# Performance work log

Measured on AMD Instinct MI355X. Metric: run time of the kernel, lower is better.

## Reference

```python
import jax, jax.numpy as jnp
import numpy as np

B, T, D, H = 1, 2049, 1024, 16
HD = D // H                      # head_dim = 64
MAX_SEQ = 1025
L = 2 * MAX_SEQ - 1              # = T (required by the module's relative shift)

def setup_inputs() -> dict:
    key = jax.random.key(0)
    ks = jax.random.split(key, 12)
    s = 0.02
    return {
        'q': jax.random.normal(ks[0], (B, T, D), dtype=jnp.float32),
        'k': jax.random.normal(ks[1], (B, T, D), dtype=jnp.float32),
        'v': jax.random.normal(ks[2], (B, T, D), dtype=jnp.float32),
        'mask': jnp.tril(jnp.ones((1, 1, T, T), dtype=jnp.int32)),  # causal
        'Wq_w': jax.random.normal(ks[3], (D, D), dtype=jnp.float32) * s,
        'Wq_b': jnp.zeros((D,), dtype=jnp.float32),
        'Wk_w': jax.random.normal(ks[4], (D, D), dtype=jnp.float32) * s,
        'Wk_b': jnp.zeros((D,), dtype=jnp.float32),
        'Wv_w': jax.random.normal(ks[5], (D, D), dtype=jnp.float32) * s,
        'Wv_b': jnp.zeros((D,), dtype=jnp.float32),
        'Er': jax.random.normal(ks[6], (L, HD), dtype=jnp.float32),
        'Wo_w': jax.random.normal(ks[7], (D, D), dtype=jnp.float32) * s,
        'Wo_b': jnp.zeros((D,), dtype=jnp.float32),
    }

def reference(q, k, v, mask, Wq_w, Wq_b, Wk_w, Wk_b, Wv_w, Wv_b, Er, Wo_w, Wo_b):
    b, t, d = q.shape
    def proj(x, w, bias):
        # nn.Linear: x @ W^T + b ; then (B,T,H,HD) -> (B,H,T,HD)
        return (x @ w.T + bias).reshape(b, t, H, HD).transpose(0, 2, 1, 3)
    qh = proj(q, Wq_w, Wq_b)
    kh = proj(k, Wk_w, Wk_b)
    vh = proj(v, Wv_w, Wv_b)
    scores = jnp.einsum('bhtd,bhsd->bhts', qh, kh)          # (B,H,T,T)
    QEr = jnp.einsum('bhtd,ld->bhtl', qh, Er)               # (B,H,T,L) with L == T
    # _relative_shift: pad a zero row on seq dim then drop first row ->
    # row i becomes QEr row i+1, last row zeros (faithful to torch code)
    rel = jnp.concatenate([QEr[:, :, 1:, :], jnp.zeros_like(QEr[:, :, :1, :])], axis=2)
    scores = scores + rel
    scores = jnp.where(mask[:, :, :t, :t] == 0, -jnp.inf, scores)
    attn = jax.nn.softmax(scores / (HD ** 0.5), axis=-1)
    ctx = jnp.einsum('bhts,bhsd->bthd', attn, vh).reshape(b, t, d)
    return ctx @ Wo_w.T + Wo_b
```

## Files before the change

### kernel.cpp

```cpp
#include <hip/hip_runtime.h>
#include <hip/hip_bf16.h>
#include <math.h>

constexpr int T_SEQ = 2049;
constexpr int D_MODEL = 1024;
constexpr int N_HEAD = 16;
constexpr int HEAD_DIM = 64;
constexpr int VT_STRIDE = 2112;
constexpr int T1_ROWS = 1152;

typedef __attribute__((ext_vector_type(8))) short short8;
typedef __attribute__((ext_vector_type(4))) short short4v;
typedef __attribute__((ext_vector_type(4))) float floatx4;

__device__ inline void load_lds16(const void* g, void* l) {
  __builtin_amdgcn_global_load_lds(
      (const __attribute__((address_space(1))) unsigned int*)g,
      (__attribute__((address_space(3))) unsigned int*)l, 16, 0, 0);
}

__device__ inline short8 cvt8_bf16(const float* p) {
  float4 a = *(const float4*)p, b = *(const float4*)(p + 4);
  __hip_bfloat16 t[8] = {__float2bfloat16(a.x), __float2bfloat16(a.y),
                         __float2bfloat16(a.z), __float2bfloat16(a.w),
                         __float2bfloat16(b.x), __float2bfloat16(b.y),
                         __float2bfloat16(b.z), __float2bfloat16(b.w)};
  return *(const short8*)t;
}

__device__ inline float bf2f(__hip_bfloat16 x) { return __bfloat162float(x); }

__global__ __launch_bounds__(256) void cast_all(
    const float* __restrict__ q, const float* __restrict__ k,
    const float* __restrict__ v, const float* __restrict__ wq,
    const float* __restrict__ wk, const float* __restrict__ wv,
    const float* __restrict__ er, const float* __restrict__ wo,
    __hip_bfloat16* __restrict__ qo, __hip_bfloat16* __restrict__ ko,
    __hip_bfloat16* __restrict__ vo, __hip_bfloat16* __restrict__ wqo,
    __hip_bfloat16* __restrict__ wko, __hip_bfloat16* __restrict__ wvo,
    __hip_bfloat16* __restrict__ ero, __hip_bfloat16* __restrict__ woo) {
  const int z = blockIdx.y;
  const float* in;
  __hip_bfloat16* out;
  int n;
  switch (z) {
    case 0: in = q; out = qo; n = T_SEQ * D_MODEL; break;
    case 1: in = k; out = ko; n = T_SEQ * D_MODEL; break;
    case 2: in = v; out = vo; n = T_SEQ * D_MODEL; break;
    case 3: in = wq; out = wqo; n = D_MODEL * D_MODEL; break;
    case 4: in = wk; out = wko; n = D_MODEL * D_MODEL; break;
    case 5: in = wv; out = wvo; n = D_MODEL * D_MODEL; break;
    case 6: in = er; out = ero; n = T_SEQ * HEAD_DIM; break;
    default: in = wo; out = woo; n = D_MODEL * D_MODEL; break;
  }
  const int i = (blockIdx.x * 256 + threadIdx.x) * 8;
  if (i + 8 > n) return;
  *(short8*)(out + i) = cvt8_bf16(in + i);
}

__global__ __launch_bounds__(512) void qkv_gemm8(
    const __hip_bfloat16* __restrict__ qbf, const __hip_bfloat16* __restrict__ kbf,
    const __hip_bfloat16* __restrict__ vbf, const __hip_bfloat16* __restrict__ wqb,
    const __hip_bfloat16* __restrict__ wkb, const __hip_bfloat16* __restrict__ wvb,
    const float* __restrict__ bq, const float* __restrict__ bk,
    const float* __restrict__ bv, __hip_bfloat16* __restrict__ qpr,
    __hip_bfloat16* __restrict__ kpr, __hip_bfloat16* __restrict__ vt,
    const float* __restrict__ er, __hip_bfloat16* __restrict__ er_bf) {
  const int d = blockIdx.x;
  const int tid = threadIdx.x;
  if (d >= 408) {
    const int i = ((d - 408) * 512 + tid) * 8;
    if (i + 8 <= T_SEQ * HEAD_DIM) *(short8*)(er_bf + i) = cvt8_bf16(er + i);
    return;
  }
  int x, p;
  if (d < 384) {
    const int g = d >> 6, rem = d & 63;
    x = rem >> 3;
    p = g * 8 + (rem & 7);
  } else {
    const int t = d - 384;
    p = 48 + (t >> 3);
    x = t & 7;
  }
  const int y = p % 17, z = p / 17;

  constexpr int K = D_MODEL, BK = 32, NS = K / BK;
  __shared__ __align__(16) char smem[32768];

  const short* A = (const short*)(z == 0 ? qbf : z == 1 ? kbf : vbf);
  const short* W = (const short*)(z == 0 ? wqb : z == 1 ? wkb : wvb);
  const float* bias = z == 0 ? bq : z == 1 ? bk : bv;

  const int wave = tid >> 6, lane = tid & 63;
  const int col = lane & 15, quad = lane >> 4;
  const int wm = wave >> 2, wn = wave & 3;
  const int m0 = y * 128, n0 = x * 128;

  const int srow = wave * 16 + (lane >> 2);
  const int sch = (lane & 3) ^ ((srow >> 1) & 3);
  const int am = min(m0 + srow, T_SEQ - 1);

#define STG(K0, BUF)                                                        \
  {                                                                         \
    load_lds16(A + (size_t)am * K + (K0) + sch * 8,                         \
               smem + (BUF)*8192 + wave * 1024);                            \
    load_lds16(W + (size_t)(n0 + srow) * K + (K0) + sch * 8,                \
               smem + 16384 + (BUF)*8192 + wave * 1024);                    \
  }

  floatx4 acc[4][2];
#pragma unroll
  for (int i = 0; i < 4; i++)
#pragma unroll
    for (int j = 0; j < 2; j++) acc[i][j] = (floatx4){0.f, 0.f, 0.f, 0.f};

  STG(0, 0)
  int buf = 0;
  for (int k0 = 0; k0 < K; k0 += BK, buf ^= 1) {
    if (k0 + BK < K) {
      STG(k0 + BK, buf ^ 1)
      asm volatile("s_waitcnt vmcnt(2)" ::: "memory");
    } else {
      asm volatile("s_waitcnt vmcnt(0)" ::: "memory");
    }
    __builtin_amdgcn_s_barrier();

    const __hip_bfloat16* as = (const __hip_bfloat16*)(smem + buf * 8192);
    const __hip_bfloat16* bs = (const __hip_bfloat16*)(smem + 16384 + buf * 8192);
    short8 af[4], bfr[2];
#pragma unroll
    for (int t = 0; t < 4; t++) {
      const int ra = wm * 64 + t * 16 + col;
      af[t] = *(const short8*)(as + ra * 32 + ((quad ^ ((ra >> 1) & 3)) * 8));
    }
#pragma unroll
    for (int t = 0; t < 2; t++) {
      const int rb = wn * 32 + t * 16 + col;
      bfr[t] = *(const short8*)(bs + rb * 32 + ((quad ^ ((rb >> 1) & 3)) * 8));
    }
#pragma unroll
    for (int mt = 0; mt < 4; mt++)
#pragma unroll
      for (int nt = 0; nt < 2; nt++)
        acc[mt][nt] = __builtin_amdgcn_mfma_f32_16x16x32_bf16(af[mt], bfr[nt],
                                                              acc[mt][nt], 0, 0, 0);
    asm volatile("" ::: "memory");
    __builtin_amdgcn_s_barrier();
  }
#undef STG

  if (z == 2) {
    short* Tt = (short*)smem;
#pragma unroll
    for (int mt = 0; mt < 4; mt++) {
      const int mb = wm * 16 + mt * 4 + quad;
#pragma unroll
      for (int nt = 0; nt < 2; nt++) {
        const int n = wn * 32 + nt * 16 + col;
        const float bb = bias[n0 + n];
        __hip_bfloat16 pk[4];
#pragma unroll
        for (int r = 0; r < 4; r++) pk[r] = __float2bfloat16(acc[mt][nt][r] + bb);
        *(short4v*)((char*)Tt + n * 256 + ((mb ^ (n & 15)) << 3)) =
            *(const short4v*)pk;
      }
    }
    __syncthreads();
    if (tid < 256) {
      const int n_loc = tid >> 1, half = tid & 1;
      if (m0 + half * 64 < VT_STRIDE) {
        const int ng = n0 + n_loc;
        __hip_bfloat16* dst = vt +
                              ((size_t)(ng >> 6) * HEAD_DIM + (ng & 63)) * VT_STRIDE +
                              m0 + half * 64;
#pragma unroll
        for (int c = 0; c < 8; c++) {
          short4v lo = *(const short4v*)((char*)Tt + n_loc * 256 +
                                         (((half * 16 + 2 * c) ^ (n_loc & 15)) << 3));
          short4v hi = *(const short4v*)((char*)Tt + n_loc * 256 +
                                         (((half * 16 + 2 * c + 1) ^ (n_loc & 15)) << 3));
          short8 o8 = {lo[0], lo[1], lo[2], lo[3], hi[0], hi[1], hi[2], hi[3]};
          *(short8*)((short*)dst + c * 8) = o8;
        }
      }
    }
    return;
  }

  __hip_bfloat16* C = z == 0 ? qpr : kpr;
#pragma unroll
  for (int mt = 0; mt < 4; mt++) {
#pragma unroll
    for (int r = 0; r < 4; r++) {
      const int m = m0 + wm * 64 + mt * 16 + quad * 4 + r;
      if (m >= T_SEQ) continue;
#pragma unroll
      for (int nt = 0; nt < 2; nt++) {
        const int n = n0 + wn * 32 + nt * 16 + col;
        const float val = acc[mt][nt][r] + bias[n];
        const int h = n >> 6, hd = n & 63;
        C[((size_t)h * T_SEQ + m) * HEAD_DIM + hd] = __float2bfloat16(val);
      }
    }
  }
}

__global__ __launch_bounds__(256) void out_gemm(
    const __hip_bfloat16* __restrict__ ctxb, const __hip_bfloat16* __restrict__ wob,
    const float* __restrict__ bias, float* __restrict__ out) {
  const int d = blockIdx.x;
  int x, p;
  if (d < 512) {
    const int g = d >> 7, rem = d & 127;
    x = rem >> 3;
    p = g * 8 + (rem & 7);
  } else {
    p = 32;
    x = d - 512;
  }
  const int m0 = p * 64, n0 = x * 64;

  constexpr int K = D_MODEL, BK = 32;
  __shared__ __align__(16) char smem[16384];

  const int tid = threadIdx.x;
  const int wave = tid >> 6, lane = tid & 63;
  const int col = lane & 15, quad = lane >> 4;
  const int wm = wave >> 1, wn = wave & 1;

  const int srow = wave * 16 + (lane >> 2);
  const int sch = (lane & 3) ^ ((srow >> 1) & 3);
  const int am = min(m0 + srow, T_SEQ - 1);
  const short* A = (const short*)ctxb;
  const short* W = (const short*)wob;

#define STG(K0, BUF)                                                        \
  {                                                                         \
    load_lds16(A + (size_t)am * K + (K0) + sch * 8,                         \
               smem + (BUF)*4096 + wave * 1024);                            \
    load_lds16(W + (size_t)(n0 + srow) * K + (K0) + sch * 8,                \
               smem + 8192 + (BUF)*4096 + wave * 1024);                     \
  }

  floatx4 acc[2][2];
#pragma unroll
  for (int i = 0; i < 2; i++)
#pragma unroll
    for (int j = 0; j < 2; j++) acc[i][j] = (floatx4){0.f, 0.f, 0.f, 0.f};

  STG(0, 0)
  int buf = 0;
  for (int k0 = 0; k0 < K; k0 += BK, buf ^= 1) {
    if (k0 + BK < K) {
      STG(k0 + BK, buf ^ 1)
      asm volatile("s_waitcnt vmcnt(2)" ::: "memory");
    } else {
      asm volatile("s_waitcnt vmcnt(0)" ::: "memory");
    }
    __builtin_amdgcn_s_barrier();

    const __hip_bfloat16* as = (const __hip_bfloat16*)(smem + buf * 4096);
    const __hip_bfloat16* bs = (const __hip_bfloat16*)(smem + 8192 + buf * 4096);
    short8 af[2], bfr[2];
#pragma unroll
    for (int t = 0; t < 2; t++) {
      const int ra = wm * 32 + t * 16 + col;
      af[t] = *(const short8*)(as + ra * 32 + ((quad ^ ((ra >> 1) & 3)) * 8));
    }
#pragma unroll
    for (int t = 0; t < 2; t++) {
      const int rb = wn * 32 + t * 16 + col;
      bfr[t] = *(const short8*)(bs + rb * 32 + ((quad ^ ((rb >> 1) & 3)) * 8));
    }
#pragma unroll
    for (int mt = 0; mt < 2; mt++)
#pragma unroll
      for (int nt = 0; nt < 2; nt++)
        acc[mt][nt] = __builtin_amdgcn_mfma_f32_16x16x32_bf16(af[mt], bfr[nt],
                                                              acc[mt][nt], 0, 0, 0);
    asm volatile("" ::: "memory");
    __builtin_amdgcn_s_barrier();
  }
#undef STG

#pragma unroll
  for (int mt = 0; mt < 2; mt++) {
#pragma unroll
    for (int r = 0; r < 4; r++) {
      const int m = m0 + wm * 32 + mt * 16 + quad * 4 + r;
      if (m >= T_SEQ) continue;
#pragma unroll
      for (int nt = 0; nt < 2; nt++) {
        const int n = n0 + wn * 32 + nt * 16 + col;
        out[(size_t)m * D_MODEL + n] = acc[mt][nt][r] + bias[n];
      }
    }
  }
}

__global__ __launch_bounds__(512, 4) void flash_attn(
    const __hip_bfloat16* __restrict__ qh, const __hip_bfloat16* __restrict__ kh,
    const __hip_bfloat16* __restrict__ er, const __hip_bfloat16* __restrict__ vt,
    __hip_bfloat16* __restrict__ ctx, __hip_bfloat16* __restrict__ O0,
    __hip_bfloat16* __restrict__ O1, float* __restrict__ l0g,
    float* __restrict__ l1g) {
  __shared__ __align__(16) __hip_bfloat16 Ks[2][64 * 128];
  __shared__ __align__(16) __hip_bfloat16 Vs[2][64 * 64];
  __shared__ __align__(16) __hip_bfloat16 Ps[8][1024];

  const int tid = threadIdx.x;
  const int id = blockIdx.x + 26 * blockIdx.y;
  const int slot = id >> 3;
  const int h = (id & 7) + 8 * (slot >= 26);
  const int b = 25 - (slot >= 26 ? slot - 26 : slot);

  const int qt = (b < 8) ? b : 8 + ((b - 8) >> 1);
  const int tq0 = qt * 128;
  const int jmax = min(tq0 + 127, T_SEQ - 1) >> 6;
  int j0, j1;
  bool alt;
  if (b < 8) {
    j0 = 0; j1 = jmax; alt = false;
  } else {
    const int mid = (jmax + 1) >> 1;
    alt = (b - 8) & 1;
    j0 = alt ? mid : 0;
    j1 = alt ? jmax : mid - 1;
  }

  const int wave = tid >> 6;
  const int lane = tid & 63;
  const int col = lane & 15;
  const int quad = lane >> 4;

  const short* qplane = (const short*)(qh + (size_t)h * T_SEQ * HEAD_DIM);
  const short* kplane = (const short*)(kh + (size_t)h * T_SEQ * HEAD_DIM);
  const short* eplane = (const short*)er;
  const short* vplane = (const short*)(vt + (size_t)h * HEAD_DIM * VT_STRIDE);

  const int t_abs = tq0 + wave * 16 + col;
  const int tload = min(t_abs, T_SEQ - 1);
  const bool hiz = (t_abs >= T_SEQ - 1);
  short8 aq[4];
#pragma unroll
  for (int kc = 0; kc < 4; kc++) {
    short8 v = *(const short8*)(qplane + (size_t)tload * 64 + kc * 32 + quad * 8);
    if (kc >= 2 && hiz) v = (short8){0, 0, 0, 0, 0, 0, 0, 0};
    aq[kc] = v;
  }

  floatx4 o[4];
  float l_lane = 0.f;
#pragma unroll
  for (int i = 0; i < 4; i++) o[i] = (floatx4){0.f, 0.f, 0.f, 0.f};

  const int tstrip = tq0 + wave * 16;
  __hip_bfloat16* psw = &Ps[wave][0];

#define STAGE_TILE(JJ, BUF)                                                        \
  {                                                                                \
    const int s0_ = (JJ) * 64;                                                     \
    _Pragma("unroll") for (int ii = 0; ii < 2; ii++) {                             \
      const int i_ = wave * 2 + ii;                                                \
      const int r_ = i_ * 4 + (lane >> 4);                                         \
      const int sl_ = lane & 15;                                                   \
      const int g_ = (sl_ & 8) | ((sl_ ^ (r_ & 7)) & 7);                           \
      const int s_ = min(s0_ + r_, T_SEQ - 1);                                     \
      const short* src_ = (g_ < 8) ? (kplane + (size_t)s_ * 64 + g_ * 8)           \
                                   : (eplane + (size_t)s_ * 64 + (g_ - 8) * 8);    \
      load_lds16(src_, (char*)&Ks[BUF][0] + i_ * 1024);                            \
    }                                                                              \
    {                                                                              \
      const int d_ = wave * 8 + (lane >> 3);                                       \
      const int sl_ = lane & 7;                                                    \
      const int g_ = sl_ ^ (d_ & 7);                                               \
      load_lds16(vplane + (size_t)d_ * VT_STRIDE + s0_ + g_ * 8,                   \
                 (char*)&Vs[BUF][0] + wave * 1024);                                \
    }                                                                              \
  }

  STAGE_TILE(j0, 0)
  int buf = 0;

  for (int j = j0; j <= j1; ++j, buf ^= 1) {
    __syncthreads();
    if (j < j1) STAGE_TILE(j + 1, buf ^ 1)

    const int s0 = j * 64;
    if (s0 > tstrip + 15) continue;

    const __hip_bfloat16* ks = &Ks[buf][0];
    const __hip_bfloat16* vs = &Vs[buf][0];

    floatx4 sacc[4];
    __builtin_amdgcn_s_setprio(1);
#pragma unroll
    for (int st = 0; st < 4; st++) {
      floatx4 c = {0.f, 0.f, 0.f, 0.f};
      const int row = st * 16 + col;
#pragma unroll
      for (int kc = 0; kc < 4; kc++) {
        const int ch = kc * 4 + quad;
        const int slot2 = (ch & 8) | ((ch ^ (row & 7)) & 7);
        short8 ka = *(const short8*)(ks + row * 128 + slot2 * 8);
        c = __builtin_amdgcn_mfma_f32_16x16x32_bf16(ka, aq[kc], c, 0, 0, 0);
      }
      sacc[st] = c;
    }
    __builtin_amdgcn_s_setprio(0);

    if (s0 + 63 > tstrip) {
#pragma unroll
      for (int st = 0; st < 4; st++) {
        const int sbase = s0 + st * 16 + quad * 4;
#pragma unroll
        for (int r = 0; r < 4; r++)
          if (sbase + r > t_abs) sacc[st][r] = -INFINITY;
      }
    }

    float rs = 0.f;
#pragma unroll
    for (int st = 0; st < 4; st++)
#pragma unroll
      for (int r = 0; r < 4; r++) {
        const float pql = __expf(sacc[st][r] * 0.125f);
        sacc[st][r] = pql;
        rs += pql;
      }
    l_lane += rs;

#pragma unroll
    for (int st = 0; st < 4; st++) {
      __hip_bfloat16 pb[4];
#pragma unroll
      for (int r = 0; r < 4; r++) pb[r] = __float2bfloat16(sacc[st][r]);
      const int kcA = st >> 1;
      const int quadA = (st & 1) * 2 + (quad >> 1);
      const int off = ((kcA * 4 + quadA) * 16 + col) * 8 + (quad & 1) * 4;
      *(short4v*)(psw + off) = *(const short4v*)pb;
    }
    short8 pa[2];
#pragma unroll
    for (int kc = 0; kc < 2; kc++)
      pa[kc] = *(const short8*)(psw + ((kc * 4 + quad) * 16 + col) * 8);

    __builtin_amdgcn_s_setprio(1);
#pragma unroll
    for (int nt = 0; nt < 4; nt++) {
      const int row = nt * 16 + col;
#pragma unroll
      for (int kc = 0; kc < 2; kc++) {
        const int slot2 = (kc * 4 + quad) ^ (row & 7);
        short8 vb = *(const short8*)(vs + row * 64 + slot2 * 8);
        o[nt] = __builtin_amdgcn_mfma_f32_16x16x32_bf16(pa[kc], vb, o[nt], 0, 0, 0);
      }
    }
    __builtin_amdgcn_s_setprio(0);
  }

  l_lane += __shfl_xor(l_lane, 16, 64);
  l_lane += __shfl_xor(l_lane, 32, 64);

  if (b < 8) {
    const float linv = 1.0f / l_lane;
    float linv_r[4];
#pragma unroll
    for (int r = 0; r < 4; r++) linv_r[r] = __shfl(linv, quad * 4 + r, 64);
#pragma unroll
    for (int r = 0; r < 4; r++) {
      const int t = tstrip + quad * 4 + r;
#pragma unroll
      for (int nt = 0; nt < 4; nt++)
        ctx[(size_t)t * D_MODEL + h * 64 + nt * 16 + col] =
            __float2bfloat16(o[nt][r] * linv_r[r]);
    }
  } else {
    if (lane < 16) {
      const int t = tstrip + lane;
      if (t < T_SEQ) {
        if (!alt)
          l0g[h * T1_ROWS + (t - 1024)] = l_lane;
        else
          l1g[h * T1_ROWS + (t - 1024)] = l_lane;
      }
    }
#pragma unroll
    for (int r = 0; r < 4; r++) {
      const int t = tstrip + quad * 4 + r;
      if (t < T_SEQ) {
        __hip_bfloat16* dst = (!alt ? O0 : O1) + (size_t)(t - 1024) * D_MODEL;
#pragma unroll
        for (int nt = 0; nt < 4; nt++)
          dst[h * 64 + nt * 16 + col] = __float2bfloat16(o[nt][r]);
      }
    }
  }
}

__global__ __launch_bounds__(256) void finalize(
    const __hip_bfloat16* __restrict__ O0, const __hip_bfloat16* __restrict__ O1,
    const float* __restrict__ l0g, const float* __restrict__ l1g,
    __hip_bfloat16* __restrict__ ctx) {
  const int idx = blockIdx.x * 256 + threadIdx.x;
  const int tr = idx >> 7;
  const int t = 1024 + tr;
  if (t >= T_SEQ) return;
  const int ch = idx & 127;
  const int h = ch >> 3;

  const float l = l0g[h * T1_ROWS + tr] + l1g[h * T1_ROWS + tr];
  const __hip_bfloat16* a = O0 + (size_t)tr * D_MODEL + ch * 8;
  const __hip_bfloat16* bsrc = O1 + (size_t)tr * D_MODEL + ch * 8;
  const float inv = 1.0f / l;
  __hip_bfloat16 outv[8];
#pragma unroll
  for (int i = 0; i < 8; i++)
    outv[i] = __float2bfloat16((bf2f(a[i]) + bf2f(bsrc[i])) * inv);
  *(short8*)(ctx + (size_t)t * D_MODEL + ch * 8) = *(const short8*)outv;
}

extern "C" void kernel_launch(void* const* d_in, const int* in_sizes, int n_in,
                              void* d_out, int out_size, void* d_ws, size_t ws_size,
                              hipStream_t stream) {
  const float* q = (const float*)d_in[0];
  const float* k = (const float*)d_in[1];
  const float* v = (const float*)d_in[2];
  const float* Wq_w = (const float*)d_in[4];
  const float* Wq_b = (const float*)d_in[5];
  const float* Wk_w = (const float*)d_in[6];
  const float* Wk_b = (const float*)d_in[7];
  const float* Wv_w = (const float*)d_in[8];
  const float* Wv_b = (const float*)d_in[9];
  const float* Er = (const float*)d_in[10];
  const float* Wo_w = (const float*)d_in[11];
  const float* Wo_b = (const float*)d_in[12];
  float* out = (float*)d_out;

  char* ws = (char*)d_ws;
  const size_t sz_plane = (size_t)T_SEQ * D_MODEL * 2;
  const size_t sz_w = (size_t)D_MODEL * D_MODEL * 2;
  const size_t sz_vt = (size_t)N_HEAD * HEAD_DIM * VT_STRIDE * 2;
  const size_t sz_er = (size_t)T_SEQ * HEAD_DIM * 2;
  const size_t sz_Op = (size_t)T1_ROWS * D_MODEL * 2;
  const size_t sz_l = (size_t)N_HEAD * T1_ROWS * 4;

  __hip_bfloat16* qbf = (__hip_bfloat16*)ws;
  __hip_bfloat16* kbf = (__hip_bfloat16*)(ws + sz_plane);
  __hip_bfloat16* vbf = (__hip_bfloat16*)(ws + 2 * sz_plane);
  __hip_bfloat16* wqb = (__hip_bfloat16*)(ws + 3 * sz_plane);
  __hip_bfloat16* wkb = (__hip_bfloat16*)(ws + 3 * sz_plane + sz_w);
  __hip_bfloat16* wvb = (__hip_bfloat16*)(ws + 3 * sz_plane + 2 * sz_w);
  char* hi = ws + 3 * sz_plane + 3 * sz_w;
  __hip_bfloat16* qpr = (__hip_bfloat16*)hi;
  __hip_bfloat16* kpr = (__hip_bfloat16*)(hi + sz_plane);
  __hip_bfloat16* vt = (__hip_bfloat16*)(hi + 2 * sz_plane);
  __hip_bfloat16* er_bf = (__hip_bfloat16*)(hi + 2 * sz_plane + sz_vt);
  __hip_bfloat16* wob = (__hip_bfloat16*)(hi + 2 * sz_plane + sz_vt + sz_er);

  __hip_bfloat16* ctxb = (__hip_bfloat16*)ws;
  __hip_bfloat16* O0 = (__hip_bfloat16*)(ws + sz_plane);
  __hip_bfloat16* O1 = (__hip_bfloat16*)(ws + sz_plane + sz_Op);
  float* l0g = (float*)(ws + sz_plane + 2 * sz_Op);
  float* l1g = (float*)(ws + sz_plane + 2 * sz_Op + sz_l);

  const dim3 blk(256);

  cast_all<<<dim3(1025, 8), blk, 0, stream>>>(q, k, v, Wq_w, Wk_w, Wv_w, Er, Wo_w,
                                              qbf, kbf, vbf, wqb, wkb, wvb, er_bf,
                                              wob);

  qkv_gemm8<<<dim3(441), dim3(512), 0, stream>>>(
      qbf, kbf, vbf, wqb, wkb, wvb, Wq_b, Wk_b, Wv_b, qpr, kpr, vt, Er, er_bf);

  flash_attn<<<dim3(26, N_HEAD), dim3(512), 0, stream>>>(qpr, kpr, er_bf, vt, ctxb,
                                                         O0, O1, l0g, l1g);

  finalize<<<dim3((1025 * 128 + 255) / 256), blk, 0, stream>>>(O0, O1, l0g, l1g,
                                                               ctxb);

  out_gemm<<<dim3(528), blk, 0, stream>>>(ctxb, wob, Wo_b, out);
}
```

Before: 180.8 us.

## Fuse split-KV finalize into flash attention via atomic ticket merge

Removes the separate finalize kernel. Each split-KV flash-attention block takes an atomic ticket per (head, query tile), and the second block to finish combines its partial output with the other block's stored partial and normalizer, then writes ctx directly. Ticket reset is folded into the cast kernel, and the redundant Er conversion blocks are dropped from the QKV GEMM launch. This saves one kernel launch and a pass over the partial buffers, in exchange for a threadfence, an atomic and extra tail work in the last-finishing blocks.

Measured after the change: 269.3 us. +49.0%, slower.

```diff
diff --git a/kernel.cpp b/kernel.cpp
--- a/kernel.cpp
+++ b/kernel.cpp
@@ -8,6 +8,7 @@
 constexpr int HEAD_DIM = 64;
 constexpr int VT_STRIDE = 2112;
 constexpr int T1_ROWS = 1152;
+constexpr int N_TICKETS = 144;
 
 typedef __attribute__((ext_vector_type(8))) short short8;
 typedef __attribute__((ext_vector_type(4))) short short4v;
@@ -38,7 +39,8 @@
     __hip_bfloat16* __restrict__ qo, __hip_bfloat16* __restrict__ ko,
     __hip_bfloat16* __restrict__ vo, __hip_bfloat16* __restrict__ wqo,
     __hip_bfloat16* __restrict__ wko, __hip_bfloat16* __restrict__ wvo,
-    __hip_bfloat16* __restrict__ ero, __hip_bfloat16* __restrict__ woo) {
+    __hip_bfloat16* __restrict__ ero, __hip_bfloat16* __restrict__ woo,
+    int* __restrict__ tickets) {
   const int z = blockIdx.y;
   const float* in;
   __hip_bfloat16* out;
@@ -50,7 +52,11 @@
     case 3: in = wq; out = wqo; n = D_MODEL * D_MODEL; break;
     case 4: in = wk; out = wko; n = D_MODEL * D_MODEL; break;
     case 5: in = wv; out = wvo; n = D_MODEL * D_MODEL; break;
-    case 6: in = er; out = ero; n = T_SEQ * HEAD_DIM; break;
+    case 6:
+      if (blockIdx.x == 1024 && threadIdx.x < N_TICKETS)
+        tickets[threadIdx.x] = 0;
+      in = er; out = ero; n = T_SEQ * HEAD_DIM;
+      break;
     default: in = wo; out = woo; n = D_MODEL * D_MODEL; break;
   }
   const int i = (blockIdx.x * 256 + threadIdx.x) * 8;
@@ -64,15 +70,9 @@
     const __hip_bfloat16* __restrict__ wkb, const __hip_bfloat16* __restrict__ wvb,
     const float* __restrict__ bq, const float* __restrict__ bk,
     const float* __restrict__ bv, __hip_bfloat16* __restrict__ qpr,
-    __hip_bfloat16* __restrict__ kpr, __hip_bfloat16* __restrict__ vt,
-    const float* __restrict__ er, __hip_bfloat16* __restrict__ er_bf) {
+    __hip_bfloat16* __restrict__ kpr, __hip_bfloat16* __restrict__ vt) {
   const int d = blockIdx.x;
   const int tid = threadIdx.x;
-  if (d >= 408) {
-    const int i = ((d - 408) * 512 + tid) * 8;
-    if (i + 8 <= T_SEQ * HEAD_DIM) *(short8*)(er_bf + i) = cvt8_bf16(er + i);
-    return;
-  }
   int x, p;
   if (d < 384) {
     const int g = d >> 6, rem = d & 63;
@@ -85,7 +85,7 @@
   }
   const int y = p % 17, z = p / 17;
 
-  constexpr int K = D_MODEL, BK = 32, NS = K / BK;
+  constexpr int K = D_MODEL, BK = 32;
   __shared__ __align__(16) char smem[32768];
 
   const short* A = (const short*)(z == 0 ? qbf : z == 1 ? kbf : vbf);
@@ -304,10 +304,11 @@
     const __hip_bfloat16* __restrict__ er, const __hip_bfloat16* __restrict__ vt,
     __hip_bfloat16* __restrict__ ctx, __hip_bfloat16* __restrict__ O0,
     __hip_bfloat16* __restrict__ O1, float* __restrict__ l0g,
-    float* __restrict__ l1g) {
+    float* __restrict__ l1g, int* __restrict__ tickets) {
   __shared__ __align__(16) __hip_bfloat16 Ks[2][64 * 128];
   __shared__ __align__(16) __hip_bfloat16 Vs[2][64 * 64];
   __shared__ __align__(16) __hip_bfloat16 Ps[8][1024];
+  __shared__ int sold;
 
   const int tid = threadIdx.x;
   const int id = blockIdx.x + 26 * blockIdx.y;
@@ -479,46 +480,53 @@
   } else {
     if (lane < 16) {
       const int t = tstrip + lane;
-      if (t < T_SEQ) {
-        if (!alt)
-          l0g[h * T1_ROWS + (t - 1024)] = l_lane;
-        else
-          l1g[h * T1_ROWS + (t - 1024)] = l_lane;
-      }
+      if (t < T_SEQ)
+        (alt ? l1g : l0g)[h * T1_ROWS + (t - 1024)] = l_lane;
     }
 #pragma unroll
     for (int r = 0; r < 4; r++) {
       const int t = tstrip + quad * 4 + r;
       if (t < T_SEQ) {
-        __hip_bfloat16* dst = (!alt ? O0 : O1) + (size_t)(t - 1024) * D_MODEL;
+        __hip_bfloat16* dst = (alt ? O1 : O0) + (size_t)(t - 1024) * D_MODEL;
 #pragma unroll
         for (int nt = 0; nt < 4; nt++)
           dst[h * 64 + nt * 16 + col] = __float2bfloat16(o[nt][r]);
       }
     }
-  }
-}
-
-__global__ __launch_bounds__(256) void finalize(
-    const __hip_bfloat16* __restrict__ O0, const __hip_bfloat16* __restrict__ O1,
-    const float* __restrict__ l0g, const float* __restrict__ l1g,
-    __hip_bfloat16* __restrict__ ctx) {
-  const int idx = blockIdx.x * 256 + threadIdx.x;
-  const int tr = idx >> 7;
-  const int t = 1024 + tr;
-  if (t >= T_SEQ) return;
-  const int ch = idx & 127;
-  const int h = ch >> 3;
-
-  const float l = l0g[h * T1_ROWS + tr] + l1g[h * T1_ROWS + tr];
-  const __hip_bfloat16* a = O0 + (size_t)tr * D_MODEL + ch * 8;
-  const __hip_bfloat16* bsrc = O1 + (size_t)tr * D_MODEL + ch * 8;
-  const float inv = 1.0f / l;
-  __hip_bfloat16 outv[8];
-#pragma unroll
-  for (int i = 0; i < 8; i++)
-    outv[i] = __float2bfloat16((bf2f(a[i]) + bf2f(bsrc[i])) * inv);
-  *(short8*)(ctx + (size_t)t * D_MODEL + ch * 8) = *(const short8*)outv;
+    __threadfence();
+    __syncthreads();
+    if (tid == 0) sold = atomicAdd(&tickets[h * 9 + (qt - 8)], 1);
+    __syncthreads();
+    if (sold == 1) {
+      __threadfence();
+      const float* lother = alt ? l0g : l1g;
+      const __hip_bfloat16* Oother = alt ? O0 : O1;
+      float lt = 1.f;
+      {
+        const int t = tstrip + col;
+        if (t < T_SEQ) lt = l_lane + lother[h * T1_ROWS + (t - 1024)];
+      }
+      const float linv = 1.0f / lt;
+      float linv_r[4];
+#pragma unroll
+      for (int r = 0; r < 4; r++) linv_r[r] = __shfl(linv, quad * 4 + r, 64);
+#pragma unroll
+      for (int r = 0; r < 4; r++) {
+        const int t = tstrip + quad * 4 + r;
+        if (t < T_SEQ) {
+          const __hip_bfloat16* osrc = Oother + (size_t)(t - 1024) * D_MODEL;
+#pragma unroll
+          for (int nt = 0; nt < 4; nt++) {
+            const int c = h * 64 + nt * 16 + col;
+            const float own = bf2f(__float2bfloat16(o[nt][r]));
+            const float oth = bf2f(osrc[c]);
+            ctx[(size_t)t * D_MODEL + c] =
+                __float2bfloat16((own + oth) * linv_r[r]);
+          }
+        }
+      }
+    }
+  }
 }
 
 extern "C" void kernel_launch(void* const* d_in, const int* in_sizes, int n_in,
@@ -558,6 +566,7 @@
   __hip_bfloat16* vt = (__hip_bfloat16*)(hi + 2 * sz_plane);
   __hip_bfloat16* er_bf = (__hip_bfloat16*)(hi + 2 * sz_plane + sz_vt);
   __hip_bfloat16* wob = (__hip_bfloat16*)(hi + 2 * sz_plane + sz_vt + sz_er);
+  int* tickets = (int*)(hi + 2 * sz_plane + sz_vt + sz_er + sz_w);
 
   __hip_bfloat16* ctxb = (__hip_bfloat16*)ws;
   __hip_bfloat16* O0 = (__hip_bfloat16*)(ws + sz_plane);
@@ -569,16 +578,13 @@
 
   cast_all<<<dim3(1025, 8), blk, 0, stream>>>(q, k, v, Wq_w, Wk_w, Wv_w, Er, Wo_w,
                                               qbf, kbf, vbf, wqb, wkb, wvb, er_bf,
-                                              wob);
-
-  qkv_gemm8<<<dim3(441), dim3(512), 0, stream>>>(
-      qbf, kbf, vbf, wqb, wkb, wvb, Wq_b, Wk_b, Wv_b, qpr, kpr, vt, Er, er_bf);
-
-  flash_attn<<<dim3(26, N_HEAD), dim3(512), 0, stream>>>(qpr, kpr, er_bf, vt, ctxb,
-                                                         O0, O1, l0g, l1g);
-
-  finalize<<<dim3((1025 * 128 + 255) / 256), blk, 0, stream>>>(O0, O1, l0g, l1g,
-                                                               ctxb);
+                                              wob, tickets);
+
+  qkv_gemm8<<<dim3(408), dim3(512), 0, stream>>>(
+      qbf, kbf, vbf, wqb, wkb, wvb, Wq_b, Wk_b, Wv_b, qpr, kpr, vt);
+
+  flash_attn<<<dim3(26, N_HEAD), dim3(512), 0, stream>>>(
+      qpr, kpr, er_bf, vt, ctxb, O0, O1, l0g, l1g, tickets);
 
   out_gemm<<<dim3(528), blk, 0, stream>>>(ctxb, wob, Wo_b, out);
 }
```

## Fuse split-KV finalize merge into output projection GEMM A-tile loading

Applied to the files above, without the earlier changes.

Removes the separate finalize kernel and instead has out_gemm blocks covering rows >= 1024 load both partial attention outputs and their row sums directly. These blocks normalize and convert the partials in registers, then write them to LDS through a register-staged software pipeline. This removes one launch and the ctx write/read round trip for the second half of rows. In exchange, those blocks use synchronous register loads instead of async global-to-LDS loads and read two planes plus the l arrays redundantly for each N tile.

New measurement: 185.5 us. 1.03x slower.

```diff
diff --git a/kernel.cpp b/kernel.cpp
--- a/kernel.cpp
+++ b/kernel.cpp
@@ -85,7 +85,7 @@
   }
   const int y = p % 17, z = p / 17;
 
-  constexpr int K = D_MODEL, BK = 32, NS = K / BK;
+  constexpr int K = D_MODEL, BK = 32;
   __shared__ __align__(16) char smem[32768];
 
   const short* A = (const short*)(z == 0 ? qbf : z == 1 ? kbf : vbf);
@@ -207,7 +207,9 @@
 }
 
 __global__ __launch_bounds__(256) void out_gemm(
-    const __hip_bfloat16* __restrict__ ctxb, const __hip_bfloat16* __restrict__ wob,
+    const __hip_bfloat16* __restrict__ ctxb, const __hip_bfloat16* __restrict__ O0,
+    const __hip_bfloat16* __restrict__ O1, const float* __restrict__ l0g,
+    const float* __restrict__ l1g, const __hip_bfloat16* __restrict__ wob,
     const float* __restrict__ bias, float* __restrict__ out) {
   const int d = blockIdx.x;
   int x, p;
@@ -220,8 +222,9 @@
     x = d - 512;
   }
   const int m0 = p * 64, n0 = x * 64;
-
-  constexpr int K = D_MODEL, BK = 32;
+  const bool merge = (m0 >= 1024);
+
+  constexpr int K = D_MODEL, BK = 32, NS = K / BK;
   __shared__ __align__(16) char smem[16384];
 
   const int tid = threadIdx.x;
@@ -232,9 +235,16 @@
   const int srow = wave * 16 + (lane >> 2);
   const int sch = (lane & 3) ^ ((srow >> 1) & 3);
   const int am = min(m0 + srow, T_SEQ - 1);
-  const short* A = (const short*)ctxb;
-  const short* W = (const short*)wob;
-
+
+  floatx4 acc[2][2];
+#pragma unroll
+  for (int i = 0; i < 2; i++)
+#pragma unroll
+    for (int j = 0; j < 2; j++) acc[i][j] = (floatx4){0.f, 0.f, 0.f, 0.f};
+
+  if (!merge) {
+    const short* A = (const short*)ctxb;
+    const short* W = (const short*)wob;
 #define STG(K0, BUF)                                                        \
   {                                                                         \
     load_lds16(A + (size_t)am * K + (K0) + sch * 8,                         \
@@ -242,47 +252,105 @@
     load_lds16(W + (size_t)(n0 + srow) * K + (K0) + sch * 8,                \
                smem + 8192 + (BUF)*4096 + wave * 1024);                     \
   }
-
-  floatx4 acc[2][2];
-#pragma unroll
-  for (int i = 0; i < 2; i++)
-#pragma unroll
-    for (int j = 0; j < 2; j++) acc[i][j] = (floatx4){0.f, 0.f, 0.f, 0.f};
-
-  STG(0, 0)
-  int buf = 0;
-  for (int k0 = 0; k0 < K; k0 += BK, buf ^= 1) {
-    if (k0 + BK < K) {
-      STG(k0 + BK, buf ^ 1)
-      asm volatile("s_waitcnt vmcnt(2)" ::: "memory");
-    } else {
-      asm volatile("s_waitcnt vmcnt(0)" ::: "memory");
-    }
-    __builtin_amdgcn_s_barrier();
-
-    const __hip_bfloat16* as = (const __hip_bfloat16*)(smem + buf * 4096);
-    const __hip_bfloat16* bs = (const __hip_bfloat16*)(smem + 8192 + buf * 4096);
-    short8 af[2], bfr[2];
-#pragma unroll
-    for (int t = 0; t < 2; t++) {
-      const int ra = wm * 32 + t * 16 + col;
-      af[t] = *(const short8*)(as + ra * 32 + ((quad ^ ((ra >> 1) & 3)) * 8));
-    }
-#pragma unroll
-    for (int t = 0; t < 2; t++) {
-      const int rb = wn * 32 + t * 16 + col;
-      bfr[t] = *(const short8*)(bs + rb * 32 + ((quad ^ ((rb >> 1) & 3)) * 8));
-    }
-#pragma unroll
-    for (int mt = 0; mt < 2; mt++)
-#pragma unroll
-      for (int nt = 0; nt < 2; nt++)
-        acc[mt][nt] = __builtin_amdgcn_mfma_f32_16x16x32_bf16(af[mt], bfr[nt],
-                                                              acc[mt][nt], 0, 0, 0);
-    asm volatile("" ::: "memory");
-    __builtin_amdgcn_s_barrier();
-  }
+    STG(0, 0)
+    int buf = 0;
+    for (int k0 = 0; k0 < K; k0 += BK, buf ^= 1) {
+      if (k0 + BK < K) {
+        STG(k0 + BK, buf ^ 1)
+        asm volatile("s_waitcnt vmcnt(2)" ::: "memory");
+      } else {
+        asm volatile("s_waitcnt vmcnt(0)" ::: "memory");
+      }
+      __builtin_amdgcn_s_barrier();
+
+      const __hip_bfloat16* as = (const __hip_bfloat16*)(smem + buf * 4096);
+      const __hip_bfloat16* bs = (const __hip_bfloat16*)(smem + 8192 + buf * 4096);
+      short8 af[2], bfr[2];
+#pragma unroll
+      for (int t = 0; t < 2; t++) {
+        const int ra = wm * 32 + t * 16 + col;
+        af[t] = *(const short8*)(as + ra * 32 + ((quad ^ ((ra >> 1) & 3)) * 8));
+      }
+#pragma unroll
+      for (int t = 0; t < 2; t++) {
+        const int rb = wn * 32 + t * 16 + col;
+        bfr[t] = *(const short8*)(bs + rb * 32 + ((quad ^ ((rb >> 1) & 3)) * 8));
+      }
+#pragma unroll
+      for (int mt = 0; mt < 2; mt++)
+#pragma unroll
+        for (int nt = 0; nt < 2; nt++)
+          acc[mt][nt] = __builtin_amdgcn_mfma_f32_16x16x32_bf16(af[mt], bfr[nt],
+                                                                acc[mt][nt], 0, 0, 0);
+      asm volatile("" ::: "memory");
+      __builtin_amdgcn_s_barrier();
+    }
 #undef STG
+  } else {
+    const int tr = am - 1024;
+    const short* O0s = (const short*)O0;
+    const short* O1s = (const short*)O1;
+    const short* Ws = (const short*)wob;
+    short8 rA0, rA1, rW, SA, SW;
+    float rl0, rl1;
+#define LOADM(K0)                                                           \
+  {                                                                         \
+    const int kb = (K0) + sch * 8;                                          \
+    rA0 = *(const short8*)(O0s + (size_t)tr * K + kb);                      \
+    rA1 = *(const short8*)(O1s + (size_t)tr * K + kb);                      \
+    rl0 = l0g[(kb >> 6) * T1_ROWS + tr];                                    \
+    rl1 = l1g[(kb >> 6) * T1_ROWS + tr];                                    \
+    rW = *(const short8*)(Ws + (size_t)(n0 + srow) * K + (K0) + sch * 8);   \
+  }
+#define CVTM()                                                              \
+  {                                                                         \
+    const float inv = 1.0f / (rl0 + rl1);                                   \
+    __hip_bfloat16 t8[8];                                                   \
+    _Pragma("unroll") for (int e = 0; e < 8; e++) t8[e] = __float2bfloat16( \
+        (bf2f(((const __hip_bfloat16*)&rA0)[e]) +                           \
+         bf2f(((const __hip_bfloat16*)&rA1)[e])) * inv);                    \
+    SA = *(const short8*)t8;                                                \
+    SW = rW;                                                                \
+  }
+    LOADM(0)
+    CVTM()
+    LOADM(BK)
+    int buf = 0;
+    for (int s = 0; s < NS; ++s, buf ^= 1) {
+      *(short8*)(smem + buf * 4096 + wave * 1024 + (lane << 4)) = SA;
+      *(short8*)(smem + 8192 + buf * 4096 + wave * 1024 + (lane << 4)) = SW;
+      asm volatile("s_waitcnt lgkmcnt(0)" ::: "memory");
+      __builtin_amdgcn_sched_barrier(0);
+      __builtin_amdgcn_s_barrier();
+
+      const __hip_bfloat16* as = (const __hip_bfloat16*)(smem + buf * 4096);
+      const __hip_bfloat16* bs = (const __hip_bfloat16*)(smem + 8192 + buf * 4096);
+      short8 af[2], bfr[2];
+#pragma unroll
+      for (int t = 0; t < 2; t++) {
+        const int ra = wm * 32 + t * 16 + col;
+        af[t] = *(const short8*)(as + ra * 32 + ((quad ^ ((ra >> 1) & 3)) * 8));
+      }
+#pragma unroll
+      for (int t = 0; t < 2; t++) {
+        const int rb = wn * 32 + t * 16 + col;
+        bfr[t] = *(const short8*)(bs + rb * 32 + ((quad ^ ((rb >> 1) & 3)) * 8));
+      }
+#pragma unroll
+      for (int mt = 0; mt < 2; mt++)
+#pragma unroll
+        for (int nt = 0; nt < 2; nt++)
+          acc[mt][nt] = __builtin_amdgcn_mfma_f32_16x16x32_bf16(af[mt], bfr[nt],
+                                                                acc[mt][nt], 0, 0, 0);
+      if (s + 1 < NS) {
+        __builtin_amdgcn_sched_barrier(0);
+        CVTM()
+        if (s + 2 < NS) LOADM((s + 2) * BK)
+      }
+    }
+#undef LOADM
+#undef CVTM
+  }
 
 #pragma unroll
   for (int mt = 0; mt < 2; mt++) {
@@ -499,28 +567,6 @@
   }
 }
 
-__global__ __launch_bounds__(256) void finalize(
-    const __hip_bfloat16* __restrict__ O0, const __hip_bfloat16* __restrict__ O1,
-    const float* __restrict__ l0g, const float* __restrict__ l1g,
-    __hip_bfloat16* __restrict__ ctx) {
-  const int idx = blockIdx.x * 256 + threadIdx.x;
-  const int tr = idx >> 7;
-  const int t = 1024 + tr;
-  if (t >= T_SEQ) return;
-  const int ch = idx & 127;
-  const int h = ch >> 3;
-
-  const float l = l0g[h * T1_ROWS + tr] + l1g[h * T1_ROWS + tr];
-  const __hip_bfloat16* a = O0 + (size_t)tr * D_MODEL + ch * 8;
-  const __hip_bfloat16* bsrc = O1 + (size_t)tr * D_MODEL + ch * 8;
-  const float inv = 1.0f / l;
-  __hip_bfloat16 outv[8];
-#pragma unroll
-  for (int i = 0; i < 8; i++)
-    outv[i] = __float2bfloat16((bf2f(a[i]) + bf2f(bsrc[i])) * inv);
-  *(short8*)(ctx + (size_t)t * D_MODEL + ch * 8) = *(const short8*)outv;
-}
-
 extern "C" void kernel_launch(void* const* d_in, const int* in_sizes, int n_in,
                               void* d_out, int out_size, void* d_ws, size_t ws_size,
                               hipStream_t stream) {
@@ -577,8 +623,5 @@
   flash_attn<<<dim3(26, N_HEAD), dim3(512), 0, stream>>>(qpr, kpr, er_bf, vt, ctxb,
                                                          O0, O1, l0g, l1g);
 
-  finalize<<<dim3((1025 * 128 + 255) / 256), blk, 0, stream>>>(O0, O1, l0g, l1g,
-                                                               ctxb);
-
-  out_gemm<<<dim3(528), blk, 0, stream>>>(ctxb, wob, Wo_b, out);
+  out_gemm<<<dim3(528), blk, 0, stream>>>(ctxb, O0, O1, l0g, l1g, wob, Wo_b, out);
 }
```

## Rebalance flash-attention work with finer split-KV partitions and table-driven scheduling

Applied to the files above, without the earlier changes.

Replaces the fixed split of query tiles (first 8 tiles whole, the rest split in two along KV) with a lookup table of 33 work slots per head. Tiles from 768 onward are split into two or three KV partitions, and the slots are issued in a chosen longest-first order. The grid grows from 26x16 to 33x16 blocks so per-block work is more even across CUs. In exchange, more rows need partial outputs written and merged, and finalize now reduces up to three partials over 1281 rows.

Measured after the change: 176.1 us. 1.03x faster.

```diff
diff --git a/kernel.cpp b/kernel.cpp
--- a/kernel.cpp
+++ b/kernel.cpp
@@ -7,11 +7,27 @@
 constexpr int N_HEAD = 16;
 constexpr int HEAD_DIM = 64;
 constexpr int VT_STRIDE = 2112;
-constexpr int T1_ROWS = 1152;
+constexpr int T2_ROWS = 1281;
 
 typedef __attribute__((ext_vector_type(8))) short short8;
 typedef __attribute__((ext_vector_type(4))) short short4v;
 typedef __attribute__((ext_vector_type(4))) float floatx4;
+
+__device__ const int d_qt[33] = {0, 1, 2, 3, 4,  5,  6,  6,  7,  7,  8,
+                                 8, 9, 9, 10, 10, 11, 11, 12, 12, 12, 13,
+                                 13, 13, 14, 14, 14, 15, 15, 15, 16, 16, 16};
+__device__ const int d_pt[33] = {0, 0, 0, 0, 0, 0, 0, 1, 0, 1, 0,
+                                 1, 0, 1, 0, 1, 0, 1, 0, 1, 2, 0,
+                                 1, 2, 0, 1, 2, 0, 1, 2, 0, 1, 2};
+__device__ const int d_j0[33] = {0, 0, 0, 0, 0,  0,  0, 7, 0, 8, 0,
+                                 9, 0, 10, 0, 11, 0, 12, 0, 8, 17, 0,
+                                 9, 18, 0, 10, 20, 0, 10, 21, 0, 11, 22};
+__device__ const int d_j1[33] = {1, 3, 5, 7, 9,  11, 6, 13, 7, 15, 8,
+                                 17, 9, 19, 10, 21, 11, 23, 7, 16, 25, 8,
+                                 17, 27, 9, 19, 29, 9, 20, 31, 10, 21, 32};
+__device__ const int d_ord[33] = {5, 16, 17, 14, 15, 28, 29, 30, 31, 32, 4,
+                                  12, 13, 23, 24, 25, 26, 27, 10, 11, 19, 20,
+                                  21, 22, 3, 8, 9, 18, 6, 7, 2, 1, 0};
 
 __device__ inline void load_lds16(const void* g, void* l) {
   __builtin_amdgcn_global_load_lds(
@@ -85,7 +101,7 @@
   }
   const int y = p % 17, z = p / 17;
 
-  constexpr int K = D_MODEL, BK = 32, NS = K / BK;
+  constexpr int K = D_MODEL, BK = 32;
   __shared__ __align__(16) char smem[32768];
 
   const short* A = (const short*)(z == 0 ? qbf : z == 1 ? kbf : vbf);
@@ -302,32 +318,23 @@
 __global__ __launch_bounds__(512, 4) void flash_attn(
     const __hip_bfloat16* __restrict__ qh, const __hip_bfloat16* __restrict__ kh,
     const __hip_bfloat16* __restrict__ er, const __hip_bfloat16* __restrict__ vt,
-    __hip_bfloat16* __restrict__ ctx, __hip_bfloat16* __restrict__ O0,
-    __hip_bfloat16* __restrict__ O1, float* __restrict__ l0g,
-    float* __restrict__ l1g) {
+    __hip_bfloat16* __restrict__ ctx, __hip_bfloat16* __restrict__ Obase,
+    float* __restrict__ lbase) {
   __shared__ __align__(16) __hip_bfloat16 Ks[2][64 * 128];
   __shared__ __align__(16) __hip_bfloat16 Vs[2][64 * 64];
   __shared__ __align__(16) __hip_bfloat16 Ps[8][1024];
 
   const int tid = threadIdx.x;
-  const int id = blockIdx.x + 26 * blockIdx.y;
-  const int slot = id >> 3;
-  const int h = (id & 7) + 8 * (slot >= 26);
-  const int b = 25 - (slot >= 26 ? slot - 26 : slot);
-
-  const int qt = (b < 8) ? b : 8 + ((b - 8) >> 1);
+  const int id = blockIdx.x + 33 * blockIdx.y;
+  const int g = id >> 3;
+  const int h = (id & 7) + 8 * (g >= 33);
+  const int sraw = (g >= 33) ? g - 33 : g;
+  const int slot = d_ord[sraw];
+  const int qt = d_qt[slot];
+  const int part = d_pt[slot];
+  const bool single = (slot < 6);
+  const int j0 = d_j0[slot], j1 = d_j1[slot];
   const int tq0 = qt * 128;
-  const int jmax = min(tq0 + 127, T_SEQ - 1) >> 6;
-  int j0, j1;
-  bool alt;
-  if (b < 8) {
-    j0 = 0; j1 = jmax; alt = false;
-  } else {
-    const int mid = (jmax + 1) >> 1;
-    alt = (b - 8) & 1;
-    j0 = alt ? mid : 0;
-    j1 = alt ? jmax : mid - 1;
-  }
 
   const int wave = tid >> 6;
   const int lane = tid & 63;
@@ -463,7 +470,7 @@
   l_lane += __shfl_xor(l_lane, 16, 64);
   l_lane += __shfl_xor(l_lane, 32, 64);
 
-  if (b < 8) {
+  if (single) {
     const float linv = 1.0f / l_lane;
     float linv_r[4];
 #pragma unroll
@@ -477,20 +484,17 @@
             __float2bfloat16(o[nt][r] * linv_r[r]);
     }
   } else {
+    __hip_bfloat16* Op = Obase + (size_t)part * T2_ROWS * D_MODEL;
+    float* lp = lbase + part * (N_HEAD * T2_ROWS);
     if (lane < 16) {
       const int t = tstrip + lane;
-      if (t < T_SEQ) {
-        if (!alt)
-          l0g[h * T1_ROWS + (t - 1024)] = l_lane;
-        else
-          l1g[h * T1_ROWS + (t - 1024)] = l_lane;
-      }
+      if (t < T_SEQ) lp[h * T2_ROWS + (t - 768)] = l_lane;
     }
 #pragma unroll
     for (int r = 0; r < 4; r++) {
       const int t = tstrip + quad * 4 + r;
       if (t < T_SEQ) {
-        __hip_bfloat16* dst = (!alt ? O0 : O1) + (size_t)(t - 1024) * D_MODEL;
+        __hip_bfloat16* dst = Op + (size_t)(t - 768) * D_MODEL;
 #pragma unroll
         for (int nt = 0; nt < 4; nt++)
           dst[h * 64 + nt * 16 + col] = __float2bfloat16(o[nt][r]);
@@ -500,24 +504,29 @@
 }
 
 __global__ __launch_bounds__(256) void finalize(
-    const __hip_bfloat16* __restrict__ O0, const __hip_bfloat16* __restrict__ O1,
-    const float* __restrict__ l0g, const float* __restrict__ l1g,
+    const __hip_bfloat16* __restrict__ Obase, const float* __restrict__ lbase,
     __hip_bfloat16* __restrict__ ctx) {
   const int idx = blockIdx.x * 256 + threadIdx.x;
   const int tr = idx >> 7;
-  const int t = 1024 + tr;
+  const int t = 768 + tr;
   if (t >= T_SEQ) return;
   const int ch = idx & 127;
   const int h = ch >> 3;
-
-  const float l = l0g[h * T1_ROWS + tr] + l1g[h * T1_ROWS + tr];
-  const __hip_bfloat16* a = O0 + (size_t)tr * D_MODEL + ch * 8;
-  const __hip_bfloat16* bsrc = O1 + (size_t)tr * D_MODEL + ch * 8;
+  const int np = ((t >> 7) >= 12) ? 3 : 2;
+
+  float l = 0.f;
+  float accv[8] = {0.f, 0.f, 0.f, 0.f, 0.f, 0.f, 0.f, 0.f};
+  for (int p = 0; p < np; ++p) {
+    l += lbase[p * (N_HEAD * T2_ROWS) + h * T2_ROWS + tr];
+    const __hip_bfloat16* src =
+        Obase + (size_t)p * T2_ROWS * D_MODEL + (size_t)tr * D_MODEL + ch * 8;
+#pragma unroll
+    for (int e = 0; e < 8; e++) accv[e] += bf2f(src[e]);
+  }
   const float inv = 1.0f / l;
   __hip_bfloat16 outv[8];
 #pragma unroll
-  for (int i = 0; i < 8; i++)
-    outv[i] = __float2bfloat16((bf2f(a[i]) + bf2f(bsrc[i])) * inv);
+  for (int e = 0; e < 8; e++) outv[e] = __float2bfloat16(accv[e] * inv);
   *(short8*)(ctx + (size_t)t * D_MODEL + ch * 8) = *(const short8*)outv;
 }
 
@@ -543,8 +552,7 @@
   const size_t sz_w = (size_t)D_MODEL * D_MODEL * 2;
   const size_t sz_vt = (size_t)N_HEAD * HEAD_DIM * VT_STRIDE * 2;
   const size_t sz_er = (size_t)T_SEQ * HEAD_DIM * 2;
-  const size_t sz_Op = (size_t)T1_ROWS * D_MODEL * 2;
-  const size_t sz_l = (size_t)N_HEAD * T1_ROWS * 4;
+  const size_t sz_O2 = (size_t)T2_ROWS * D_MODEL * 2;
 
   __hip_bfloat16* qbf = (__hip_bfloat16*)ws;
   __hip_bfloat16* kbf = (__hip_bfloat16*)(ws + sz_plane);
@@ -560,10 +568,8 @@
   __hip_bfloat16* wob = (__hip_bfloat16*)(hi + 2 * sz_plane + sz_vt + sz_er);
 
   __hip_bfloat16* ctxb = (__hip_bfloat16*)ws;
-  __hip_bfloat16* O0 = (__hip_bfloat16*)(ws + sz_plane);
-  __hip_bfloat16* O1 = (__hip_bfloat16*)(ws + sz_plane + sz_Op);
-  float* l0g = (float*)(ws + sz_plane + 2 * sz_Op);
-  float* l1g = (float*)(ws + sz_plane + 2 * sz_Op + sz_l);
+  __hip_bfloat16* Obase = (__hip_bfloat16*)(ws + sz_plane);
+  float* lbase = (float*)(ws + 3 * sz_plane);
 
   const dim3 blk(256);
 
@@ -574,11 +580,11 @@
   qkv_gemm8<<<dim3(441), dim3(512), 0, stream>>>(
       qbf, kbf, vbf, wqb, wkb, wvb, Wq_b, Wk_b, Wv_b, qpr, kpr, vt, Er, er_bf);
 
-  flash_attn<<<dim3(26, N_HEAD), dim3(512), 0, stream>>>(qpr, kpr, er_bf, vt, ctxb,
-                                                         O0, O1, l0g, l1g);
-
-  finalize<<<dim3((1025 * 128 + 255) / 256), blk, 0, stream>>>(O0, O1, l0g, l1g,
-                                                               ctxb);
+  flash_attn<<<dim3(33, N_HEAD), dim3(512), 0, stream>>>(qpr, kpr, er_bf, vt, ctxb,
+                                                         Obase, lbase);
+
+  finalize<<<dim3((T2_ROWS * 128 + 255) / 256), blk, 0, stream>>>(Obase, lbase,
+                                                                  ctxb);
 
   out_gemm<<<dim3(528), blk, 0, stream>>>(ctxb, wob, Wo_b, out);
 }
```
